# Kernel optimization log

Hardware: AMD Instinct MI355X
Metric: run time of the kernel (lower is better)

Reference implementation:

```python
import jax, jax.numpy as jnp
import numpy as np

B, L, C = 1, 4096, 1024
H = 16
D = C // H  # head_dim = 64


def setup_inputs() -> dict:
    key = jax.random.key(0)
    k1, k2, k3 = jax.random.split(key, 3)
    scale_in = 1.0 / np.sqrt(C)
    return {
        "x": jax.random.normal(k1, (B, L, C), dtype=jnp.float32),
        "Wqkv": jax.random.normal(k2, (C, 3 * C), dtype=jnp.float32) * scale_in,
        "bqkv": jnp.zeros((3 * C,), dtype=jnp.float32),
        "Wout": jax.random.normal(k3, (C, C), dtype=jnp.float32) * scale_in,
        "bout": jnp.zeros((C,), dtype=jnp.float32),
    }


def reference(x, Wqkv, bqkv, Wout, bout):
    Bx, Lx, Cx = x.shape
    qkv = x @ Wqkv + bqkv                             # [B, L, 3C]
    qkv = qkv.reshape(Bx, Lx, 3, H, D)
    qkv = jnp.transpose(qkv, (2, 0, 3, 1, 4))         # [3, B, H, L, D]
    q, k, v = qkv[0], qkv[1], qkv[2]
    scores = jnp.einsum("bhqd,bhkd->bhqk", q, k) / jnp.sqrt(jnp.float32(D))
    # causal mask: strictly upper triangle -> -inf
    causal = jnp.triu(jnp.ones((Lx, Lx), dtype=bool), k=1)
    scores = jnp.where(causal, -jnp.inf, scores)
    attn = jax.nn.softmax(scores, axis=-1)            # [B, H, L, L]
    out = jnp.einsum("bhqk,bhkd->bhqd", attn, v)      # [B, H, L, D]
    out = jnp.transpose(out, (0, 2, 1, 3)).reshape(Bx, Lx, Cx)
    return out @ Wout + bout
```

## Files before the change

kernel.cpp:

```cpp
#include <hip/hip_runtime.h>
#include <hip/hip_bf16.h>

typedef unsigned short u16;
typedef __bf16 bf16x8 __attribute__((ext_vector_type(8)));
typedef float f32x4 __attribute__((ext_vector_type(4)));

#define L_SEQ 4096
#define CDIM  1024
#define NH    16
#define HD    64
#define N_QKV 3072
#define ATT_STRIDE 72
#define TILE_HW (64 * ATT_STRIDE)

static __device__ __forceinline__ float bf2f(u16 u) {
    union { float f; unsigned int i; } v; v.i = ((unsigned int)u) << 16; return v.f;
}
static __device__ __forceinline__ u16 f2bf(float f) {
    union { float f; unsigned int i; } v; v.f = f;
    unsigned int u = v.i;
    return (u16)((u + 0x7fffu + ((u >> 16) & 1u)) >> 16);
}
static __device__ __forceinline__ float exp2_(float x) {
    return __builtin_exp2f(x);
}

static __device__ __forceinline__ f32x4 mfma16x16x32(bf16x8 a, bf16x8 b, f32x4 c) {
    return __builtin_amdgcn_mfma_f32_16x16x32_bf16(a, b, c, 0, 0, 0);
}

typedef const __attribute__((address_space(1))) unsigned int* gas_u32;
typedef __attribute__((address_space(3))) unsigned int* las_u32;
static __device__ __forceinline__ void gload_lds16(const u16* g, u16* l) {
    __builtin_amdgcn_global_load_lds((gas_u32)g, (las_u32)l, 16, 0, 0);
}

__global__ __launch_bounds__(256) void k_cast_x(const float* __restrict__ src,
                                                u16* __restrict__ dst, int n8) {
    int i = blockIdx.x * 256 + threadIdx.x;
    if (i >= n8) return;
    const float4* s = (const float4*)(src + (size_t)i * 8);
    float4 a = s[0], b = s[1];
    u16 o[8] = { f2bf(a.x), f2bf(a.y), f2bf(a.z), f2bf(a.w),
                 f2bf(b.x), f2bf(b.y), f2bf(b.z), f2bf(b.w) };
    *(uint4*)(dst + (size_t)i * 8) = *(uint4*)o;
}

__global__ __launch_bounds__(256) void k_transpose_cast(const float* __restrict__ src,
                                                        u16* __restrict__ dst,
                                                        int R, int C) {
    __shared__ u16 tile[32][33];
    int c0 = blockIdx.x * 32, r0 = blockIdx.y * 32;
    int tx = threadIdx.x & 31, ty = threadIdx.x >> 5;
#pragma unroll
    for (int i = 0; i < 32; i += 8)
        tile[ty + i][tx] = f2bf(src[(size_t)(r0 + ty + i) * C + c0 + tx]);
    __syncthreads();
#pragma unroll
    for (int i = 0; i < 32; i += 8)
        dst[(size_t)(c0 + ty + i) * R + r0 + tx] = tile[tx][ty + i];
}

template <typename OutT, int BN, bool FUSE_VT>
__global__ __launch_bounds__(256) void k_gemm_bt(const u16* __restrict__ A,
                                                 const u16* __restrict__ Bt,
                                                 const float* __restrict__ bias,
                                                 OutT* __restrict__ Cmat,
                                                 u16* __restrict__ vt,
                                                 int M, int N, int K) {
    constexpr int NI = BN / 32;
    __shared__ alignas(16) u16 As[2][128 * 32];
    __shared__ alignas(16) u16 Bs[2][BN * 32];
    int t = threadIdx.x;
    int n0 = blockIdx.x * BN, m0 = blockIdx.y * 128;
    int l = t & 63, w = t >> 6;
    int wm = (w >> 1) * 64, wn = (w & 1) * (BN / 2);
    int lr = l & 15, lq = l >> 4;

    const f32x4 vzero = {0.f, 0.f, 0.f, 0.f};
    f32x4 acc[4][NI];
#pragma unroll
    for (int mi = 0; mi < 4; mi++)
#pragma unroll
        for (int ni = 0; ni < NI; ni++) acc[mi][ni] = vzero;

    int ar = t >> 2;
    int ac = (t & 3) * 8;
    const u16* Ag = A + (size_t)(m0 + ar) * K + ac;
    const u16* Bg = Bt + (size_t)(n0 + ar) * K + ac;

    int nk = K >> 5;

    auto stage = [&](int kt, int bu) {
        int k0 = kt << 5;
        gload_lds16(Ag + k0,                  &As[bu][t * 8]);
        gload_lds16(Ag + (size_t)64 * K + k0, &As[bu][t * 8 + 64 * 32]);
        gload_lds16(Bg + k0,                  &Bs[bu][t * 8]);
        if constexpr (BN == 128)
            gload_lds16(Bg + (size_t)64 * K + k0, &Bs[bu][t * 8 + 64 * 32]);
    };

    stage(0, 0);
    __syncthreads();

    int bu = 0;
    for (int kt = 0; kt < nk; ++kt) {
        if (kt + 1 < nk) stage(kt + 1, bu ^ 1);

        bf16x8 af[4], bfr[NI];
#pragma unroll
        for (int mi = 0; mi < 4; mi++)
            af[mi] = *(const bf16x8*)&As[bu][(wm + mi * 16 + lr) * 32 + lq * 8];
#pragma unroll
        for (int ni = 0; ni < NI; ni++)
            bfr[ni] = *(const bf16x8*)&Bs[bu][(wn + ni * 16 + lr) * 32 + lq * 8];
#pragma unroll
        for (int mi = 0; mi < 4; mi++)
#pragma unroll
            for (int ni = 0; ni < NI; ni++)
                acc[mi][ni] = mfma16x16x32(af[mi], bfr[ni], acc[mi][ni]);

        __syncthreads();
        bu ^= 1;
    }

    bool vpath = FUSE_VT && (n0 >= 2 * CDIM);
    if (vpath) {
#pragma unroll
        for (int ni = 0; ni < NI; ni++) {
            int col = n0 + wn + ni * 16 + lr;
            float bv = bias[col];
            int d = col - 2 * CDIM;
#pragma unroll
            for (int mi = 0; mi < 4; mi++) {
                int row = m0 + wm + mi * 16 + lq * 4;
                union { u16 hh[4]; uint2 u2; } eo;
#pragma unroll
                for (int r = 0; r < 4; r++) eo.hh[r] = f2bf(acc[mi][ni][r] + bv);
                *(uint2*)&vt[(size_t)d * L_SEQ + row] = eo.u2;
            }
        }
    } else {
#pragma unroll
        for (int ni = 0; ni < NI; ni++) {
            int col = n0 + wn + ni * 16 + lr;
            float bv = bias[col];
#pragma unroll
            for (int mi = 0; mi < 4; mi++) {
                int row = m0 + wm + mi * 16 + lq * 4;
#pragma unroll
                for (int r = 0; r < 4; r++) {
                    float v = acc[mi][ni][r] + bv;
                    if constexpr (sizeof(OutT) == 2)
                        Cmat[(size_t)(row + r) * N + col] = f2bf(v);
                    else
                        Cmat[(size_t)(row + r) * N + col] = v;
                }
            }
        }
    }
}

__global__ __launch_bounds__(512, 4) void k_attn(const u16* __restrict__ qkv,
                                                 const u16* __restrict__ vt,
                                                 u16* __restrict__ attn) {
    __shared__ alignas(16) u16 Ks[2][2 * TILE_HW];
    __shared__ alignas(16) u16 Vs[2][2 * TILE_HW];

    int t = threadIdx.x;
    int l = t & 63, w = t >> 6;
    int g = w >> 2;
    int ww = w & 3;
    int h = blockIdx.x;
    int pair = blockIdx.y;
    int lr = l & 15, lq = l >> 4;
    int tg = t & 255;
    int row8 = tg >> 3;
    int ch = (tg & 7) * 8;
    int qloc = ww * 16 + lr;

    const f32x4 vzero = {0.f, 0.f, 0.f, 0.f};
    const u16* Kbase = qkv + (size_t)row8 * N_QKV + CDIM + h * HD + ch;
    const u16* Vbase = vt + (size_t)(h * HD + row8) * L_SEQ + ch;
    u16* KsG = Ks[g];
    u16* VsG = Vs[g];

#pragma unroll
    for (int phase = 0; phase < 2; phase++) {
        int tile = phase ? (63 - pair) : pair;
        int q0 = tile * 64;
        int nkv = tile + 1;
        int h0 = (nkv + 1) >> 1;
        int myBeg = g ? h0 : 0;
        int myCnt = g ? (nkv - h0) : h0;

        const float SC = 0.125f * 1.44269504089f;
        bf16x8 bq[2];
        {
            const u16* Qg = qkv + (size_t)(q0 + qloc) * N_QKV + h * HD + lq * 8;
            union { uint4 u; u16 hh[8]; } q0u, q1u;
            q0u.u = *(const uint4*)(Qg);
            q1u.u = *(const uint4*)(Qg + 32);
            union { bf16x8 v; __bf16 e[8]; } f0, f1;
#pragma unroll
            for (int j = 0; j < 8; j++) {
                f0.e[j] = (__bf16)(bf2f(q0u.hh[j]) * SC);
                f1.e[j] = (__bf16)(bf2f(q1u.hh[j]) * SC);
            }
            bq[0] = f0.v; bq[1] = f1.v;
        }

        f32x4 o[4];
#pragma unroll
        for (int dt = 0; dt < 4; dt++) o[dt] = vzero;
        float m_i = -1e30f, l_i = 0.f;

        uint4 rk0 = {0,0,0,0}, rk1 = {0,0,0,0}, rv0 = {0,0,0,0}, rv1 = {0,0,0,0};
        if (myCnt > 0) {
            const u16* Kg = Kbase + (size_t)(myBeg * 64) * N_QKV;
            rk0 = *(const uint4*)Kg;
            rk1 = *(const uint4*)(Kg + (size_t)32 * N_QKV);
            const u16* Vg = Vbase + myBeg * 64;
            rv0 = *(const uint4*)Vg;
            rv1 = *(const uint4*)(Vg + (size_t)32 * L_SEQ);
            *(uint4*)&KsG[row8 * ATT_STRIDE + ch]        = rk0;
            *(uint4*)&KsG[(row8 + 32) * ATT_STRIDE + ch] = rk1;
            *(uint4*)&VsG[row8 * ATT_STRIDE + ch]        = rv0;
            *(uint4*)&VsG[(row8 + 32) * ATT_STRIDE + ch] = rv1;
            if (myCnt > 1) {
                int k1 = (myBeg + 1) * 64;
                Kg = Kbase + (size_t)k1 * N_QKV;
                rk0 = *(const uint4*)Kg;
                rk1 = *(const uint4*)(Kg + (size_t)32 * N_QKV);
                Vg = Vbase + k1;
                rv0 = *(const uint4*)Vg;
                rv1 = *(const uint4*)(Vg + (size_t)32 * L_SEQ);
            }
        }
        __syncthreads();

        for (int j = 0; j < h0; ++j) {
            int cur = (j & 1) ? TILE_HW : 0;
            if (j + 1 < myCnt) {
                int nxt = TILE_HW - cur;
                *(uint4*)&KsG[nxt + row8 * ATT_STRIDE + ch]        = rk0;
                *(uint4*)&KsG[nxt + (row8 + 32) * ATT_STRIDE + ch] = rk1;
                *(uint4*)&VsG[nxt + row8 * ATT_STRIDE + ch]        = rv0;
                *(uint4*)&VsG[nxt + (row8 + 32) * ATT_STRIDE + ch] = rv1;
            }
            if (j + 2 < myCnt) {
                int k1 = (myBeg + j + 2) * 64;
                const u16* Kg = Kbase + (size_t)k1 * N_QKV;
                rk0 = *(const uint4*)Kg;
                rk1 = *(const uint4*)(Kg + (size_t)32 * N_QKV);
                const u16* Vg = Vbase + k1;
                rv0 = *(const uint4*)Vg;
                rv1 = *(const uint4*)(Vg + (size_t)32 * L_SEQ);
            }

            if (j < myCnt) {
                const u16* Kc = KsG + cur;
                const u16* Vc = VsG + cur;

                f32x4 s[4];
#pragma unroll
                for (int nt = 0; nt < 4; nt++) s[nt] = vzero;
                __builtin_amdgcn_s_setprio(1);
#pragma unroll
                for (int ks = 0; ks < 2; ks++)
#pragma unroll
                    for (int nt = 0; nt < 4; nt++) {
                        bf16x8 ak = *(const bf16x8*)&Kc[(nt * 16 + lr) * ATT_STRIDE + ks * 32 + lq * 8];
                        s[nt] = mfma16x16x32(ak, bq[ks], s[nt]);
                    }
                __builtin_amdgcn_s_setprio(0);

                bool diag = (((myBeg + j) * 64) == q0);
                float tmax = -1e30f;
                if (diag) {
#pragma unroll
                    for (int nt = 0; nt < 4; nt++)
#pragma unroll
                        for (int r = 0; r < 4; r++) {
                            float v = s[nt][r];
                            if (nt * 16 + lq * 4 + r > qloc) v = -1e30f;
                            s[nt][r] = v;
                            tmax = fmaxf(tmax, v);
                        }
                } else {
#pragma unroll
                    for (int nt = 0; nt < 4; nt++)
#pragma unroll
                        for (int r = 0; r < 4; r++) tmax = fmaxf(tmax, s[nt][r]);
                }

                if (!__all(tmax <= m_i + 11.0f)) {
                    float tq = fmaxf(tmax, __shfl_xor(tmax, 16));
                    tq = fmaxf(tq, __shfl_xor(tq, 32));
                    float mnew = fmaxf(m_i, tq);
                    float alpha = exp2_(m_i - mnew);
                    l_i *= alpha;
#pragma unroll
                    for (int dt = 0; dt < 4; dt++)
#pragma unroll
                        for (int r = 0; r < 4; r++) o[dt][r] *= alpha;
                    m_i = mnew;
                }

#pragma unroll
                for (int nt = 0; nt < 4; nt++)
#pragma unroll
                    for (int r = 0; r < 4; r++) {
                        float e = exp2_(s[nt][r] - m_i);
                        s[nt][r] = e;
                        l_i += e;
                    }

                __builtin_amdgcn_s_setprio(1);
#pragma unroll
                for (int a = 0; a < 2; a++) {
                    union { bf16x8 v; __bf16 e[8]; } bp;
#pragma unroll
                    for (int r = 0; r < 4; r++) {
                        bp.e[r]     = (__bf16)s[2 * a][r];
                        bp.e[r + 4] = (__bf16)s[2 * a + 1][r];
                    }
#pragma unroll
                    for (int dt = 0; dt < 4; dt++) {
                        union { bf16x8 v; uint2 u2[2]; } av;
                        const u16* vrow = &Vc[(dt * 16 + lr) * ATT_STRIDE + a * 32 + lq * 4];
                        av.u2[0] = *(const uint2*)(vrow);
                        av.u2[1] = *(const uint2*)(vrow + 16);
                        o[dt] = mfma16x16x32(av.v, bp.v, o[dt]);
                    }
                }
                __builtin_amdgcn_s_setprio(0);
            }
            __syncthreads();
        }

        l_i += __shfl_xor(l_i, 16);
        l_i += __shfl_xor(l_i, 32);

        float* mb1 = (float*)Ks[1];
        float* mb2 = (float*)Vs[1];
        if (g == 1) {
            float* p = mb1 + tg * 10;
            p[0] = m_i; p[1] = l_i;
#pragma unroll
            for (int r = 0; r < 4; r++) { p[2 + r] = o[0][r]; p[6 + r] = o[1][r]; }
            float* p2 = mb2 + tg * 8;
#pragma unroll
            for (int r = 0; r < 4; r++) { p2[r] = o[2][r]; p2[4 + r] = o[3][r]; }
        }
        __syncthreads();
        if (g == 0) {
            float* p = mb1 + tg * 10;
            float m1v = p[0], l1v = p[1];
            float mnew = fmaxf(m_i, m1v);
            float a0 = exp2_(m_i - mnew);
            float a1 = exp2_(m1v - mnew);
            float lm = l_i * a0 + l1v * a1;
            float* p2 = mb2 + tg * 8;
            f32x4 o1[4];
#pragma unroll
            for (int r = 0; r < 4; r++) {
                o1[0][r] = p[2 + r]; o1[1][r] = p[6 + r];
                o1[2][r] = p2[r];    o1[3][r] = p2[4 + r];
            }
            float inv = 1.0f / lm;
            int qg = q0 + qloc;
#pragma unroll
            for (int dt = 0; dt < 4; dt++) {
                union { u16 hh[4]; uint2 u2; __bf16 e[4]; } eo;
#pragma unroll
                for (int r = 0; r < 4; r++)
                    eo.e[r] = (__bf16)((o[dt][r] * a0 + o1[dt][r] * a1) * inv);
                *(uint2*)&attn[(size_t)qg * CDIM + h * HD + dt * 16 + lq * 4] = eo.u2;
            }
        }
        __syncthreads();
    }
}

extern "C" void kernel_launch(void* const* d_in, const int* in_sizes, int n_in,
                              void* d_out, int out_size, void* d_ws, size_t ws_size,
                              hipStream_t stream) {
    const float* x    = (const float*)d_in[0];
    const float* Wqkv = (const float*)d_in[1];
    const float* bqkv = (const float*)d_in[2];
    const float* Wout = (const float*)d_in[3];
    const float* bout = (const float*)d_in[4];
    float* out = (float*)d_out;

    char* ws = (char*)d_ws;
    u16* qkv   = (u16*)(ws);
    u16* xb    = (u16*)(ws + 25165824);
    u16* attn  = xb;
    u16* vt    = (u16*)(ws + 33554432);
    u16* wqkvt = (u16*)(ws + 41943040);
    u16* woutt = (u16*)(ws + 48234496);

    k_cast_x<<<dim3(2048), 256, 0, stream>>>(x, xb, 524288);
    k_transpose_cast<<<dim3(96, 32), 256, 0, stream>>>(Wqkv, wqkvt, 1024, 3072);
    k_transpose_cast<<<dim3(32, 32), 256, 0, stream>>>(Wout, woutt, 1024, 1024);
    k_gemm_bt<u16, 128, true><<<dim3(24, 32), 256, 0, stream>>>(
        xb, wqkvt, bqkv, qkv, vt, 4096, 3072, 1024);
    k_attn<<<dim3(16, 32), 512, 0, stream>>>(qkv, vt, attn);
    k_gemm_bt<float, 64, false><<<dim3(16, 32), 256, 0, stream>>>(
        attn, woutt, bout, out, nullptr, 4096, 1024, 1024);
}
```

Before: 228.2 us.

## Launch one attention block per query tile with single-buffered LDS

The attention kernel no longer pairs a short and a long query tile per block. It launches 64 tiles per head, one block each, so the grid doubles to 1024 blocks. Shared memory drops from double-buffered to single-buffered K/V tiles (halving LDS) and launch bounds rise to 8 waves per SIMD, aiming for higher occupancy. In exchange, causal load balance now relies on the hardware scheduler instead of the explicit pairing. The global-to-LDS prefetch also overlaps less, since each LDS store now sits behind a barrier.

Measured after the change: 332.2 us. +45.6%, slower.

```diff
diff --git a/kernel.cpp b/kernel.cpp
--- a/kernel.cpp
+++ b/kernel.cpp
@@ -11,7 +11,7 @@
 #define HD    64
 #define N_QKV 3072
 #define ATT_STRIDE 72
-#define TILE_HW (64 * ATT_STRIDE)
+#define ATILE1 (64 * ATT_STRIDE)
 
 static __device__ __forceinline__ float bf2f(u16 u) {
     union { float f; unsigned int i; } v; v.i = ((unsigned int)u) << 16; return v.f;
@@ -161,225 +161,199 @@
     }
 }
 
-__global__ __launch_bounds__(512, 4) void k_attn(const u16* __restrict__ qkv,
+__global__ __launch_bounds__(512, 8) void k_attn(const u16* __restrict__ qkv,
                                                  const u16* __restrict__ vt,
                                                  u16* __restrict__ attn) {
-    __shared__ alignas(16) u16 Ks[2][2 * TILE_HW];
-    __shared__ alignas(16) u16 Vs[2][2 * TILE_HW];
+    __shared__ alignas(16) u16 smem[4 * ATILE1];
 
     int t = threadIdx.x;
     int l = t & 63, w = t >> 6;
     int g = w >> 2;
     int ww = w & 3;
     int h = blockIdx.x;
-    int pair = blockIdx.y;
+    int tile = blockIdx.y;
     int lr = l & 15, lq = l >> 4;
     int tg = t & 255;
     int row8 = tg >> 3;
     int ch = (tg & 7) * 8;
     int qloc = ww * 16 + lr;
 
+    u16* KsG = smem + g * ATILE1;
+    u16* VsG = smem + 2 * ATILE1 + g * ATILE1;
+
+    int q0 = tile * 64;
+    int nkv = tile + 1;
+    int h0 = (nkv + 1) >> 1;
+    int myBeg = g ? h0 : 0;
+    int myCnt = g ? (nkv - h0) : h0;
+
     const f32x4 vzero = {0.f, 0.f, 0.f, 0.f};
     const u16* Kbase = qkv + (size_t)row8 * N_QKV + CDIM + h * HD + ch;
     const u16* Vbase = vt + (size_t)(h * HD + row8) * L_SEQ + ch;
-    u16* KsG = Ks[g];
-    u16* VsG = Vs[g];
-
-#pragma unroll
-    for (int phase = 0; phase < 2; phase++) {
-        int tile = phase ? (63 - pair) : pair;
-        int q0 = tile * 64;
-        int nkv = tile + 1;
-        int h0 = (nkv + 1) >> 1;
-        int myBeg = g ? h0 : 0;
-        int myCnt = g ? (nkv - h0) : h0;
-
-        const float SC = 0.125f * 1.44269504089f;
-        bf16x8 bq[2];
-        {
-            const u16* Qg = qkv + (size_t)(q0 + qloc) * N_QKV + h * HD + lq * 8;
-            union { uint4 u; u16 hh[8]; } q0u, q1u;
-            q0u.u = *(const uint4*)(Qg);
-            q1u.u = *(const uint4*)(Qg + 32);
-            union { bf16x8 v; __bf16 e[8]; } f0, f1;
-#pragma unroll
-            for (int j = 0; j < 8; j++) {
-                f0.e[j] = (__bf16)(bf2f(q0u.hh[j]) * SC);
-                f1.e[j] = (__bf16)(bf2f(q1u.hh[j]) * SC);
-            }
-            bq[0] = f0.v; bq[1] = f1.v;
-        }
-
-        f32x4 o[4];
-#pragma unroll
-        for (int dt = 0; dt < 4; dt++) o[dt] = vzero;
-        float m_i = -1e30f, l_i = 0.f;
-
-        uint4 rk0 = {0,0,0,0}, rk1 = {0,0,0,0}, rv0 = {0,0,0,0}, rv1 = {0,0,0,0};
-        if (myCnt > 0) {
-            const u16* Kg = Kbase + (size_t)(myBeg * 64) * N_QKV;
-            rk0 = *(const uint4*)Kg;
-            rk1 = *(const uint4*)(Kg + (size_t)32 * N_QKV);
-            const u16* Vg = Vbase + myBeg * 64;
-            rv0 = *(const uint4*)Vg;
-            rv1 = *(const uint4*)(Vg + (size_t)32 * L_SEQ);
+
+    const float SC = 0.125f * 1.44269504089f;
+    bf16x8 bq[2];
+    {
+        const u16* Qg = qkv + (size_t)(q0 + qloc) * N_QKV + h * HD + lq * 8;
+        union { uint4 u; u16 hh[8]; } q0u, q1u;
+        q0u.u = *(const uint4*)(Qg);
+        q1u.u = *(const uint4*)(Qg + 32);
+        union { bf16x8 v; __bf16 e[8]; } f0, f1;
+#pragma unroll
+        for (int j = 0; j < 8; j++) {
+            f0.e[j] = (__bf16)(bf2f(q0u.hh[j]) * SC);
+            f1.e[j] = (__bf16)(bf2f(q1u.hh[j]) * SC);
+        }
+        bq[0] = f0.v; bq[1] = f1.v;
+    }
+
+    f32x4 o[4];
+#pragma unroll
+    for (int dt = 0; dt < 4; dt++) o[dt] = vzero;
+    float m_i = -1e30f, l_i = 0.f;
+
+    uint4 rk0 = {0,0,0,0}, rk1 = {0,0,0,0}, rv0 = {0,0,0,0}, rv1 = {0,0,0,0};
+    auto ldkv = [&](int kvt) {
+        const u16* Kg = Kbase + (size_t)(kvt * 64) * N_QKV;
+        rk0 = *(const uint4*)Kg;
+        rk1 = *(const uint4*)(Kg + (size_t)32 * N_QKV);
+        const u16* Vg = Vbase + kvt * 64;
+        rv0 = *(const uint4*)Vg;
+        rv1 = *(const uint4*)(Vg + (size_t)32 * L_SEQ);
+    };
+    if (myCnt > 0) ldkv(myBeg);
+
+    for (int j = 0; j < h0; ++j) {
+        bool act = j < myCnt;
+        if (act) {
             *(uint4*)&KsG[row8 * ATT_STRIDE + ch]        = rk0;
             *(uint4*)&KsG[(row8 + 32) * ATT_STRIDE + ch] = rk1;
             *(uint4*)&VsG[row8 * ATT_STRIDE + ch]        = rv0;
             *(uint4*)&VsG[(row8 + 32) * ATT_STRIDE + ch] = rv1;
-            if (myCnt > 1) {
-                int k1 = (myBeg + 1) * 64;
-                Kg = Kbase + (size_t)k1 * N_QKV;
-                rk0 = *(const uint4*)Kg;
-                rk1 = *(const uint4*)(Kg + (size_t)32 * N_QKV);
-                Vg = Vbase + k1;
-                rv0 = *(const uint4*)Vg;
-                rv1 = *(const uint4*)(Vg + (size_t)32 * L_SEQ);
-            }
         }
         __syncthreads();
 
-        for (int j = 0; j < h0; ++j) {
-            int cur = (j & 1) ? TILE_HW : 0;
-            if (j + 1 < myCnt) {
-                int nxt = TILE_HW - cur;
-                *(uint4*)&KsG[nxt + row8 * ATT_STRIDE + ch]        = rk0;
-                *(uint4*)&KsG[nxt + (row8 + 32) * ATT_STRIDE + ch] = rk1;
-                *(uint4*)&VsG[nxt + row8 * ATT_STRIDE + ch]        = rv0;
-                *(uint4*)&VsG[nxt + (row8 + 32) * ATT_STRIDE + ch] = rv1;
-            }
-            if (j + 2 < myCnt) {
-                int k1 = (myBeg + j + 2) * 64;
-                const u16* Kg = Kbase + (size_t)k1 * N_QKV;
-                rk0 = *(const uint4*)Kg;
-                rk1 = *(const uint4*)(Kg + (size_t)32 * N_QKV);
-                const u16* Vg = Vbase + k1;
-                rv0 = *(const uint4*)Vg;
-                rv1 = *(const uint4*)(Vg + (size_t)32 * L_SEQ);
-            }
-
-            if (j < myCnt) {
-                const u16* Kc = KsG + cur;
-                const u16* Vc = VsG + cur;
-
-                f32x4 s[4];
-#pragma unroll
-                for (int nt = 0; nt < 4; nt++) s[nt] = vzero;
-                __builtin_amdgcn_s_setprio(1);
-#pragma unroll
-                for (int ks = 0; ks < 2; ks++)
-#pragma unroll
-                    for (int nt = 0; nt < 4; nt++) {
-                        bf16x8 ak = *(const bf16x8*)&Kc[(nt * 16 + lr) * ATT_STRIDE + ks * 32 + lq * 8];
-                        s[nt] = mfma16x16x32(ak, bq[ks], s[nt]);
+        if (j + 1 < myCnt) ldkv(myBeg + j + 1);
+
+        if (act) {
+            int kvt = myBeg + j;
+
+            f32x4 s[4];
+#pragma unroll
+            for (int nt = 0; nt < 4; nt++) s[nt] = vzero;
+            __builtin_amdgcn_s_setprio(1);
+#pragma unroll
+            for (int ks = 0; ks < 2; ks++)
+#pragma unroll
+                for (int nt = 0; nt < 4; nt++) {
+                    bf16x8 ak = *(const bf16x8*)&KsG[(nt * 16 + lr) * ATT_STRIDE + ks * 32 + lq * 8];
+                    s[nt] = mfma16x16x32(ak, bq[ks], s[nt]);
+                }
+            __builtin_amdgcn_s_setprio(0);
+
+            bool diag = (kvt == tile);
+            float tmax = -1e30f;
+            if (diag) {
+#pragma unroll
+                for (int nt = 0; nt < 4; nt++)
+#pragma unroll
+                    for (int r = 0; r < 4; r++) {
+                        float v = s[nt][r];
+                        if (nt * 16 + lq * 4 + r > qloc) v = -1e30f;
+                        s[nt][r] = v;
+                        tmax = fmaxf(tmax, v);
                     }
-                __builtin_amdgcn_s_setprio(0);
-
-                bool diag = (((myBeg + j) * 64) == q0);
-                float tmax = -1e30f;
-                if (diag) {
-#pragma unroll
-                    for (int nt = 0; nt < 4; nt++)
-#pragma unroll
-                        for (int r = 0; r < 4; r++) {
-                            float v = s[nt][r];
-                            if (nt * 16 + lq * 4 + r > qloc) v = -1e30f;
-                            s[nt][r] = v;
-                            tmax = fmaxf(tmax, v);
-                        }
-                } else {
-#pragma unroll
-                    for (int nt = 0; nt < 4; nt++)
-#pragma unroll
-                        for (int r = 0; r < 4; r++) tmax = fmaxf(tmax, s[nt][r]);
-                }
-
-                if (!__all(tmax <= m_i + 11.0f)) {
-                    float tq = fmaxf(tmax, __shfl_xor(tmax, 16));
-                    tq = fmaxf(tq, __shfl_xor(tq, 32));
-                    float mnew = fmaxf(m_i, tq);
-                    float alpha = exp2_(m_i - mnew);
-                    l_i *= alpha;
-#pragma unroll
-                    for (int dt = 0; dt < 4; dt++)
-#pragma unroll
-                        for (int r = 0; r < 4; r++) o[dt][r] *= alpha;
-                    m_i = mnew;
-                }
-
+            } else {
 #pragma unroll
                 for (int nt = 0; nt < 4; nt++)
 #pragma unroll
-                    for (int r = 0; r < 4; r++) {
-                        float e = exp2_(s[nt][r] - m_i);
-                        s[nt][r] = e;
-                        l_i += e;
-                    }
-
-                __builtin_amdgcn_s_setprio(1);
-#pragma unroll
-                for (int a = 0; a < 2; a++) {
-                    union { bf16x8 v; __bf16 e[8]; } bp;
-#pragma unroll
-                    for (int r = 0; r < 4; r++) {
-                        bp.e[r]     = (__bf16)s[2 * a][r];
-                        bp.e[r + 4] = (__bf16)s[2 * a + 1][r];
-                    }
-#pragma unroll
-                    for (int dt = 0; dt < 4; dt++) {
-                        union { bf16x8 v; uint2 u2[2]; } av;
-                        const u16* vrow = &Vc[(dt * 16 + lr) * ATT_STRIDE + a * 32 + lq * 4];
-                        av.u2[0] = *(const uint2*)(vrow);
-                        av.u2[1] = *(const uint2*)(vrow + 16);
-                        o[dt] = mfma16x16x32(av.v, bp.v, o[dt]);
-                    }
-                }
-                __builtin_amdgcn_s_setprio(0);
-            }
-            __syncthreads();
-        }
-
-        l_i += __shfl_xor(l_i, 16);
-        l_i += __shfl_xor(l_i, 32);
-
-        float* mb1 = (float*)Ks[1];
-        float* mb2 = (float*)Vs[1];
-        if (g == 1) {
-            float* p = mb1 + tg * 10;
-            p[0] = m_i; p[1] = l_i;
-#pragma unroll
-            for (int r = 0; r < 4; r++) { p[2 + r] = o[0][r]; p[6 + r] = o[1][r]; }
-            float* p2 = mb2 + tg * 8;
-#pragma unroll
-            for (int r = 0; r < 4; r++) { p2[r] = o[2][r]; p2[4 + r] = o[3][r]; }
+                    for (int r = 0; r < 4; r++) tmax = fmaxf(tmax, s[nt][r]);
+            }
+
+            if (!__all(tmax <= m_i + 11.0f)) {
+                float tq = fmaxf(tmax, __shfl_xor(tmax, 16));
+                tq = fmaxf(tq, __shfl_xor(tq, 32));
+                float mnew = fmaxf(m_i, tq);
+                float alpha = exp2_(m_i - mnew);
+                l_i *= alpha;
+#pragma unroll
+                for (int dt = 0; dt < 4; dt++)
+#pragma unroll
+                    for (int r = 0; r < 4; r++) o[dt][r] *= alpha;
+                m_i = mnew;
+            }
+
+#pragma unroll
+            for (int nt = 0; nt < 4; nt++)
+#pragma unroll
+                for (int r = 0; r < 4; r++) {
+                    float e = exp2_(s[nt][r] - m_i);
+                    s[nt][r] = e;
+                    l_i += e;
+                }
+
+            __builtin_amdgcn_s_setprio(1);
+#pragma unroll
+            for (int a = 0; a < 2; a++) {
+                union { bf16x8 v; __bf16 e[8]; } bp;
+#pragma unroll
+                for (int r = 0; r < 4; r++) {
+                    bp.e[r]     = (__bf16)s[2 * a][r];
+                    bp.e[r + 4] = (__bf16)s[2 * a + 1][r];
+                }
+#pragma unroll
+                for (int dt = 0; dt < 4; dt++) {
+                    union { bf16x8 v; uint2 u2[2]; } av;
+                    const u16* vrow = &VsG[(dt * 16 + lr) * ATT_STRIDE + a * 32 + lq * 4];
+                    av.u2[0] = *(const uint2*)(vrow);
+                    av.u2[1] = *(const uint2*)(vrow + 16);
+                    o[dt] = mfma16x16x32(av.v, bp.v, o[dt]);
+                }
+            }
+            __builtin_amdgcn_s_setprio(0);
         }
         __syncthreads();
-        if (g == 0) {
-            float* p = mb1 + tg * 10;
-            float m1v = p[0], l1v = p[1];
-            float mnew = fmaxf(m_i, m1v);
-            float a0 = exp2_(m_i - mnew);
-            float a1 = exp2_(m1v - mnew);
-            float lm = l_i * a0 + l1v * a1;
-            float* p2 = mb2 + tg * 8;
-            f32x4 o1[4];
-#pragma unroll
-            for (int r = 0; r < 4; r++) {
-                o1[0][r] = p[2 + r]; o1[1][r] = p[6 + r];
-                o1[2][r] = p2[r];    o1[3][r] = p2[4 + r];
-            }
-            float inv = 1.0f / lm;
-            int qg = q0 + qloc;
-#pragma unroll
-            for (int dt = 0; dt < 4; dt++) {
-                union { u16 hh[4]; uint2 u2; __bf16 e[4]; } eo;
-#pragma unroll
-                for (int r = 0; r < 4; r++)
-                    eo.e[r] = (__bf16)((o[dt][r] * a0 + o1[dt][r] * a1) * inv);
-                *(uint2*)&attn[(size_t)qg * CDIM + h * HD + dt * 16 + lq * 4] = eo.u2;
-            }
-        }
-        __syncthreads();
+    }
+
+    l_i += __shfl_xor(l_i, 16);
+    l_i += __shfl_xor(l_i, 32);
+
+    float* mb1 = (float*)smem;
+    float* mb2 = (float*)smem + 2560;
+    if (g == 1) {
+        float* p = mb1 + tg * 10;
+        p[0] = m_i; p[1] = l_i;
+#pragma unroll
+        for (int r = 0; r < 4; r++) { p[2 + r] = o[0][r]; p[6 + r] = o[1][r]; }
+        float* p2 = mb2 + tg * 8;
+#pragma unroll
+        for (int r = 0; r < 4; r++) { p2[r] = o[2][r]; p2[4 + r] = o[3][r]; }
+    }
+    __syncthreads();
+    if (g == 0) {
+        float* p = mb1 + tg * 10;
+        float m1v = p[0], l1v = p[1];
+        float mnew = fmaxf(m_i, m1v);
+        float a0 = exp2_(m_i - mnew);
+        float a1 = exp2_(m1v - mnew);
+        float lm = l_i * a0 + l1v * a1;
+        float* p2 = mb2 + tg * 8;
+        f32x4 o1[4];
+#pragma unroll
+        for (int r = 0; r < 4; r++) {
+            o1[0][r] = p[2 + r]; o1[1][r] = p[6 + r];
+            o1[2][r] = p2[r];    o1[3][r] = p2[4 + r];
+        }
+        float inv = 1.0f / lm;
+        int qg = q0 + qloc;
+#pragma unroll
+        for (int dt = 0; dt < 4; dt++) {
+            union { u16 hh[4]; uint2 u2; __bf16 e[4]; } eo;
+#pragma unroll
+            for (int r = 0; r < 4; r++)
+                eo.e[r] = (__bf16)((o[dt][r] * a0 + o1[dt][r] * a1) * inv);
+            *(uint2*)&attn[(size_t)qg * CDIM + h * HD + dt * 16 + lq * 4] = eo.u2;
+        }
     }
 }
 
@@ -406,7 +380,7 @@
     k_transpose_cast<<<dim3(32, 32), 256, 0, stream>>>(Wout, woutt, 1024, 1024);
     k_gemm_bt<u16, 128, true><<<dim3(24, 32), 256, 0, stream>>>(
         xb, wqkvt, bqkv, qkv, vt, 4096, 3072, 1024);
-    k_attn<<<dim3(16, 32), 512, 0, stream>>>(qkv, vt, attn);
+    k_attn<<<dim3(16, 64), 512, 0, stream>>>(qkv, vt, attn);
     k_gemm_bt<float, 64, false><<<dim3(16, 32), 256, 0, stream>>>(
         attn, woutt, bout, out, nullptr, 4096, 1024, 1024);
 }
```
